# Performance work log

Hardware: AMD Instinct MI355X
Metric: run time of the kernel (lower is better)

Reference implementation:

```python
import jax, jax.numpy as jnp
import numpy as np
import math

B, Q, K, D = 32, 2048, 2048, 128


def setup_inputs() -> dict:
    key = jax.random.key(0)
    k1, k2, k3, k4 = jax.random.split(key, 4)
    return {
        "queries": jax.random.normal(k1, (B, Q, D), dtype=jnp.float32),
        "keys": jax.random.normal(k2, (B, K, D), dtype=jnp.float32),
        "values": jax.random.normal(k3, (B, K, D), dtype=jnp.float32),
        "valid_len": jax.random.randint(k4, (B,), 0, Q, dtype=jnp.int32),
    }


def reference(queries, keys, values, valid_len):
    d = queries.shape[-1]
    # [B, Q, K] scores
    scores = jnp.einsum("bqd,bkd->bqk", queries, keys) / math.sqrt(d)
    # Faithful to source: mask is over the QUERY dim (X.size(1) of [B,Q,K]);
    # rows with q >= valid_len[b] are set entirely to -1e5 before softmax.
    row_mask = jnp.arange(scores.shape[1]) < valid_len[:, None]  # [B, Q]
    scores = jnp.where(row_mask[:, :, None], scores, -100000.0)
    attn = jax.nn.softmax(scores, axis=-1)  # dropout p=0 -> identity
    return jnp.einsum("bqk,bkv->bqv", attn, values)
```

## Files before the change

kernel.cpp:

```cpp
#include <hip/hip_runtime.h>
#include <stdint.h>

#define NB 32
#define NQ 2048
#define NKK 2048
#define DH 128

constexpr int QBLK = 256;
constexpr int KBLK = 64;
constexpr int NKT  = NKK / KBLK;
constexpr float C2 = 0.12754299817f;

typedef short short8  __attribute__((ext_vector_type(8)));
typedef float f32x4   __attribute__((ext_vector_type(4)));
typedef float f32x16  __attribute__((ext_vector_type(16)));
typedef uint32_t u32x4 __attribute__((ext_vector_type(4)));

typedef __attribute__((address_space(3))) uint32_t lds_u32_t;
typedef __attribute__((address_space(1))) const uint32_t glb_u32_t;

__device__ __forceinline__ uint16_t f2bf(float x) {
    union { float f; uint32_t u; } v; v.f = x;
    uint32_t r = v.u + 0x7fffu + ((v.u >> 16) & 1u);
    return (uint16_t)(r >> 16);
}

__device__ __forceinline__ void gload16(const void* g, void* l) {
    __builtin_amdgcn_global_load_lds((glb_u32_t*)g, (lds_u32_t*)l, 16, 0, 0);
}

__device__ __forceinline__ uint32_t cvtpk(float lo, float hi) {
    uint32_t d;
    asm("v_cvt_pk_bf16_f32 %0, %1, %2" : "=v"(d) : "v"(lo), "v"(hi));
    return d;
}

__global__ void conv_kf(const float* __restrict__ K, uint16_t* __restrict__ Kf) {
    __shared__ __align__(16) uint16_t T[64][136];
    const int bid = blockIdx.x;
    const int b = bid >> 5, kt = bid & 31;
    const int tid = threadIdx.x;
    const float* src = K + ((size_t)(b * NKK + kt * 64)) * DH;
    #pragma unroll
    for (int r = 0; r < 8; ++r) {
        int flat = r * 256 + tid;
        int row = flat >> 5;
        int c4 = (flat & 31) * 4;
        f32x4 x = *(const f32x4*)(src + (size_t)row * DH + c4);
        T[row][c4 + 0] = f2bf(x[0]);
        T[row][c4 + 1] = f2bf(x[1]);
        T[row][c4 + 2] = f2bf(x[2]);
        T[row][c4 + 3] = f2bf(x[3]);
    }
    __syncthreads();
    uint16_t* dst = Kf + (size_t)bid * 8192;
    #pragma unroll
    for (int r = 0; r < 4; ++r) {
        int c = r * 256 + tid;
        int s = c >> 6, lane = c & 63;
        int ci = s >> 3, t = s & 7;
        int mm = lane & 31, hh = lane >> 5;
        short8 v = *(const short8*)&T[ci * 32 + mm][t * 16 + hh * 8];
        *(short8*)(dst + (size_t)c * 8) = v;
    }
}

__global__ void conv_vf(const float* __restrict__ V, uint16_t* __restrict__ Vf) {
    const int bid = blockIdx.x;
    const int b = bid >> 5, kt = bid & 31;
    const int tid = threadIdx.x;
    const float* src = V + (size_t)b * NKK * DH;
    uint16_t* dst = Vf + (size_t)bid * 8192;
    #pragma unroll
    for (int r = 0; r < 4; ++r) {
        int c = r * 256 + tid;
        int s = c >> 6, lane = c & 63;
        int ci = s >> 3, nt = (s >> 1) & 3, uu = s & 1;
        int m = lane & 31, h = lane >> 5;
        int kb = kt * 64 + ci * 32 + uu * 16 + 4 * h;
        int d = nt * 32 + m;
        short8 w;
        #pragma unroll
        for (int j = 0; j < 8; ++j) {
            int key = kb + (j & 3) + 8 * (j >> 2);
            w[j] = (short)f2bf(src[(size_t)key * DH + d]);
        }
        *(short8*)(dst + (size_t)c * 8) = w;
    }
}

__global__ __launch_bounds__(256, 1)
void attn_fwd(const float* __restrict__ Qg, const uint16_t* __restrict__ Kf,
              const uint16_t* __restrict__ Vf, const int* __restrict__ VL,
              float* __restrict__ Og) {
    __shared__ __align__(16) uint8_t LB[65536];

    const int tid  = threadIdx.x;
    const int wv   = tid >> 6;
    const int lane = tid & 63;
    const int m    = lane & 31;
    const int h    = lane >> 5;

    const int bid = blockIdx.x;
    const int swz = (bid & 7) * 32 + (bid >> 3);
    const int b   = swz >> 3;
    const int qt  = swz & 7;
    const int qb0 = qt * QBLK + wv * 64;

    const int vlen = VL[b];

    short8 qf[2][8];
    #pragma unroll
    for (int qs = 0; qs < 2; ++qs) {
        const int qrow = qb0 + qs * 32 + m;
        const float qsc = (qrow < vlen) ? C2 : 0.0f;
        const float* qp = Qg + ((size_t)b * NQ + qrow) * DH;
        #pragma unroll
        for (int t = 0; t < 8; ++t) {
            const float* p = qp + t * 16 + h * 8;
            f32x4 x0 = *(const f32x4*)(p);
            f32x4 x1 = *(const f32x4*)(p + 4);
            short8 f;
            f[0] = f2bf(x0[0] * qsc); f[1] = f2bf(x0[1] * qsc);
            f[2] = f2bf(x0[2] * qsc); f[3] = f2bf(x0[3] * qsc);
            f[4] = f2bf(x1[0] * qsc); f[5] = f2bf(x1[1] * qsc);
            f[6] = f2bf(x1[2] * qsc); f[7] = f2bf(x1[3] * qsc);
            qf[qs][t] = f;
        }
    }

    f32x16 oacc[2][4];
    #pragma unroll
    for (int qs = 0; qs < 2; ++qs)
        #pragma unroll
        for (int nt = 0; nt < 4; ++nt)
            #pragma unroll
            for (int r = 0; r < 16; ++r) oacc[qs][nt][r] = 0.0f;
    float lsum[2] = {0.0f, 0.0f};

    const char* kfb = (const char*)Kf + (size_t)b * 32 * 16384;
    const char* vfb = (const char*)Vf + (size_t)b * 32 * 16384;

    auto stage = [&](int buf, int ktile) {
        const char* ks = kfb + (size_t)ktile * 16384;
        const char* vs = vfb + (size_t)ktile * 16384;
        char* kd = (char*)LB + buf * 16384;
        char* vd = (char*)LB + 32768 + buf * 16384;
        #pragma unroll
        for (int r = 0; r < 4; ++r) {
            gload16(ks + r * 4096 + tid * 16, kd + r * 4096 + tid * 16);
            gload16(vs + r * 4096 + tid * 16, vd + r * 4096 + tid * 16);
        }
    };

    stage(0, 0);
    __syncthreads();

    int cur = 0;
    for (int kt = 0; kt < NKT; ++kt) {
        if (kt + 1 < NKT) stage(cur ^ 1, kt + 1);
        const char* KTc = (const char*)LB + cur * 16384 + (size_t)lane * 16;
        const char* VTc = (const char*)LB + 32768 + cur * 16384 + (size_t)lane * 16;

        short8 pa[2][4];
        #pragma unroll
        for (int ci = 0; ci < 2; ++ci) {
            f32x16 s0, s1;
            #pragma unroll
            for (int r = 0; r < 16; ++r) { s0[r] = 0.0f; s1[r] = 0.0f; }
            #pragma unroll
            for (int t = 0; t < 8; ++t) {
                short8 kf = *(const short8*)(KTc + (ci * 8 + t) * 1024);
                s0 = __builtin_amdgcn_mfma_f32_32x32x16_bf16(kf, qf[0][t], s0, 0, 0, 0);
                s1 = __builtin_amdgcn_mfma_f32_32x32x16_bf16(kf, qf[1][t], s1, 0, 0, 0);
            }
            #pragma unroll
            for (int uu = 0; uu < 2; ++uu) {
                float p0[8], p1[8];
                #pragma unroll
                for (int j = 0; j < 8; ++j) {
                    p0[j] = __builtin_amdgcn_exp2f(s0[uu * 8 + j]);
                    p1[j] = __builtin_amdgcn_exp2f(s1[uu * 8 + j]);
                }
                lsum[0] += ((p0[0] + p0[1]) + (p0[2] + p0[3])) + ((p0[4] + p0[5]) + (p0[6] + p0[7]));
                lsum[1] += ((p1[0] + p1[1]) + (p1[2] + p1[3])) + ((p1[4] + p1[5]) + (p1[6] + p1[7]));
                union { uint32_t w[4]; short8 s; } u0, u1;
                u0.w[0] = cvtpk(p0[0], p0[1]); u0.w[1] = cvtpk(p0[2], p0[3]);
                u0.w[2] = cvtpk(p0[4], p0[5]); u0.w[3] = cvtpk(p0[6], p0[7]);
                u1.w[0] = cvtpk(p1[0], p1[1]); u1.w[1] = cvtpk(p1[2], p1[3]);
                u1.w[2] = cvtpk(p1[4], p1[5]); u1.w[3] = cvtpk(p1[6], p1[7]);
                pa[0][ci * 2 + uu] = u0.s;
                pa[1][ci * 2 + uu] = u1.s;
            }
        }

        #pragma unroll
        for (int nt = 0; nt < 4; ++nt) {
            #pragma unroll
            for (int u = 0; u < 4; ++u) {
                const int ci = u >> 1;
                const int uu = u & 1;
                short8 vfr = *(const short8*)(VTc + (ci * 8 + nt * 2 + uu) * 1024);
                oacc[0][nt] = __builtin_amdgcn_mfma_f32_32x32x16_bf16(pa[0][u], vfr, oacc[0][nt], 0, 0, 0);
                oacc[1][nt] = __builtin_amdgcn_mfma_f32_32x32x16_bf16(pa[1][u], vfr, oacc[1][nt], 0, 0, 0);
            }
        }

        __syncthreads();
        cur ^= 1;
    }

    float lt0 = lsum[0] + __shfl_xor(lsum[0], 32);
    float lt1 = lsum[1] + __shfl_xor(lsum[1], 32);
    float* op = Og + ((size_t)b * NQ + qb0) * DH;
    #pragma unroll
    for (int qs = 0; qs < 2; ++qs) {
        float ltq = qs ? lt1 : lt0;
        #pragma unroll
        for (int r = 0; r < 16; ++r) {
            const int qr = (r & 3) + 8 * (r >> 2) + 4 * h;
            float inv = 1.0f / __shfl(ltq, qr);
            #pragma unroll
            for (int nt = 0; nt < 4; ++nt)
                op[(size_t)(qs * 32 + qr) * DH + nt * 32 + m] = oacc[qs][nt][r] * inv;
        }
    }
}

extern "C" void kernel_launch(void* const* d_in, const int* in_sizes, int n_in,
                              void* d_out, int out_size, void* d_ws, size_t ws_size,
                              hipStream_t stream) {
    const float* q  = (const float*)d_in[0];
    const float* k  = (const float*)d_in[1];
    const float* v  = (const float*)d_in[2];
    const int*   vl = (const int*)d_in[3];
    float* out = (float*)d_out;

    uint16_t* Kf = (uint16_t*)d_ws;
    uint16_t* Vf = Kf + (size_t)NB * NKT * 8192;

    conv_kf<<<NB * NKT, 256, 0, stream>>>(k, Kf);
    conv_vf<<<NB * NKT, 256, 0, stream>>>(v, Vf);
    attn_fwd<<<NB * (NQ / QBLK), 256, 0, stream>>>(q, Kf, Vf, vl, out);
}
```

Baseline: 94.76 us.

## Split attention block into compute and producer waves with MFMA priority hints

Raises the block to 512 threads. Four waves do the QK and PV MFMA work, and four dedicated waves only issue the global-to-LDS staging of the next K/V tile. The compute waves also interleave the two key chunks' score MFMAs, reorder the PV loop, and raise wave priority around MFMA sections with s_setprio. The aim is to take load-issue overhead off the compute waves. In exchange, the launch-bounds change to (512,2) can force register spilling given the large accumulator state, and LDS use of 64KB per block may still cap occupancy at one block per CU.

```diff
diff --git a/kernel.cpp b/kernel.cpp
--- a/kernel.cpp
+++ b/kernel.cpp
@@ -89,7 +89,7 @@
     }
 }
 
-__global__ __launch_bounds__(256, 1)
+__global__ __launch_bounds__(512, 2)
 void attn_fwd(const float* __restrict__ Qg, const uint16_t* __restrict__ Kf,
               const uint16_t* __restrict__ Vf, const int* __restrict__ VL,
               float* __restrict__ Og) {
@@ -105,124 +105,142 @@
     const int swz = (bid & 7) * 32 + (bid >> 3);
     const int b   = swz >> 3;
     const int qt  = swz & 7;
-    const int qb0 = qt * QBLK + wv * 64;
-
-    const int vlen = VL[b];
-
-    short8 qf[2][8];
-    #pragma unroll
-    for (int qs = 0; qs < 2; ++qs) {
-        const int qrow = qb0 + qs * 32 + m;
-        const float qsc = (qrow < vlen) ? C2 : 0.0f;
-        const float* qp = Qg + ((size_t)b * NQ + qrow) * DH;
-        #pragma unroll
-        for (int t = 0; t < 8; ++t) {
-            const float* p = qp + t * 16 + h * 8;
-            f32x4 x0 = *(const f32x4*)(p);
-            f32x4 x1 = *(const f32x4*)(p + 4);
-            short8 f;
-            f[0] = f2bf(x0[0] * qsc); f[1] = f2bf(x0[1] * qsc);
-            f[2] = f2bf(x0[2] * qsc); f[3] = f2bf(x0[3] * qsc);
-            f[4] = f2bf(x1[0] * qsc); f[5] = f2bf(x1[1] * qsc);
-            f[6] = f2bf(x1[2] * qsc); f[7] = f2bf(x1[3] * qsc);
-            qf[qs][t] = f;
-        }
-    }
-
-    f32x16 oacc[2][4];
-    #pragma unroll
-    for (int qs = 0; qs < 2; ++qs)
-        #pragma unroll
-        for (int nt = 0; nt < 4; ++nt)
-            #pragma unroll
-            for (int r = 0; r < 16; ++r) oacc[qs][nt][r] = 0.0f;
-    float lsum[2] = {0.0f, 0.0f};
 
     const char* kfb = (const char*)Kf + (size_t)b * 32 * 16384;
     const char* vfb = (const char*)Vf + (size_t)b * 32 * 16384;
 
     auto stage = [&](int buf, int ktile) {
+        const int ptid = tid & 255;
         const char* ks = kfb + (size_t)ktile * 16384;
         const char* vs = vfb + (size_t)ktile * 16384;
         char* kd = (char*)LB + buf * 16384;
         char* vd = (char*)LB + 32768 + buf * 16384;
         #pragma unroll
         for (int r = 0; r < 4; ++r) {
-            gload16(ks + r * 4096 + tid * 16, kd + r * 4096 + tid * 16);
-            gload16(vs + r * 4096 + tid * 16, vd + r * 4096 + tid * 16);
+            gload16(ks + r * 4096 + ptid * 16, kd + r * 4096 + ptid * 16);
+            gload16(vs + r * 4096 + ptid * 16, vd + r * 4096 + ptid * 16);
         }
     };
 
-    stage(0, 0);
+    const int qb0 = qt * QBLK + (wv & 3) * 64;
+
+    short8 qf[2][8];
+    f32x16 oacc[2][4];
+    float lsum[2] = {0.0f, 0.0f};
+
+    if (wv < 4) {
+        const int vlen = VL[b];
+        #pragma unroll
+        for (int qs = 0; qs < 2; ++qs) {
+            const int qrow = qb0 + qs * 32 + m;
+            const float qsc = (qrow < vlen) ? C2 : 0.0f;
+            const float* qp = Qg + ((size_t)b * NQ + qrow) * DH;
+            #pragma unroll
+            for (int t = 0; t < 8; ++t) {
+                const float* p = qp + t * 16 + h * 8;
+                f32x4 x0 = *(const f32x4*)(p);
+                f32x4 x1 = *(const f32x4*)(p + 4);
+                short8 f;
+                f[0] = f2bf(x0[0] * qsc); f[1] = f2bf(x0[1] * qsc);
+                f[2] = f2bf(x0[2] * qsc); f[3] = f2bf(x0[3] * qsc);
+                f[4] = f2bf(x1[0] * qsc); f[5] = f2bf(x1[1] * qsc);
+                f[6] = f2bf(x1[2] * qsc); f[7] = f2bf(x1[3] * qsc);
+                qf[qs][t] = f;
+            }
+        }
+        #pragma unroll
+        for (int qs = 0; qs < 2; ++qs)
+            #pragma unroll
+            for (int nt = 0; nt < 4; ++nt)
+                #pragma unroll
+                for (int r = 0; r < 16; ++r) oacc[qs][nt][r] = 0.0f;
+    } else {
+        stage(0, 0);
+    }
     __syncthreads();
 
-    int cur = 0;
     for (int kt = 0; kt < NKT; ++kt) {
-        if (kt + 1 < NKT) stage(cur ^ 1, kt + 1);
-        const char* KTc = (const char*)LB + cur * 16384 + (size_t)lane * 16;
-        const char* VTc = (const char*)LB + 32768 + cur * 16384 + (size_t)lane * 16;
-
-        short8 pa[2][4];
-        #pragma unroll
-        for (int ci = 0; ci < 2; ++ci) {
-            f32x16 s0, s1;
-            #pragma unroll
-            for (int r = 0; r < 16; ++r) { s0[r] = 0.0f; s1[r] = 0.0f; }
+        const int cur = kt & 1;
+        if (wv < 4) {
+            const char* KTc = (const char*)LB + cur * 16384 + (size_t)lane * 16;
+            const char* VTc = (const char*)LB + 32768 + cur * 16384 + (size_t)lane * 16;
+
+            f32x16 s[2][2];
+            #pragma unroll
+            for (int ci = 0; ci < 2; ++ci)
+                #pragma unroll
+                for (int qs = 0; qs < 2; ++qs)
+                    #pragma unroll
+                    for (int r = 0; r < 16; ++r) s[ci][qs][r] = 0.0f;
+            __builtin_amdgcn_s_setprio(1);
             #pragma unroll
             for (int t = 0; t < 8; ++t) {
-                short8 kf = *(const short8*)(KTc + (ci * 8 + t) * 1024);
-                s0 = __builtin_amdgcn_mfma_f32_32x32x16_bf16(kf, qf[0][t], s0, 0, 0, 0);
-                s1 = __builtin_amdgcn_mfma_f32_32x32x16_bf16(kf, qf[1][t], s1, 0, 0, 0);
-            }
-            #pragma unroll
-            for (int uu = 0; uu < 2; ++uu) {
-                float p0[8], p1[8];
-                #pragma unroll
-                for (int j = 0; j < 8; ++j) {
-                    p0[j] = __builtin_amdgcn_exp2f(s0[uu * 8 + j]);
-                    p1[j] = __builtin_amdgcn_exp2f(s1[uu * 8 + j]);
+                short8 kf0 = *(const short8*)(KTc + (0 * 8 + t) * 1024);
+                short8 kf1 = *(const short8*)(KTc + (1 * 8 + t) * 1024);
+                s[0][0] = __builtin_amdgcn_mfma_f32_32x32x16_bf16(kf0, qf[0][t], s[0][0], 0, 0, 0);
+                s[0][1] = __builtin_amdgcn_mfma_f32_32x32x16_bf16(kf0, qf[1][t], s[0][1], 0, 0, 0);
+                s[1][0] = __builtin_amdgcn_mfma_f32_32x32x16_bf16(kf1, qf[0][t], s[1][0], 0, 0, 0);
+                s[1][1] = __builtin_amdgcn_mfma_f32_32x32x16_bf16(kf1, qf[1][t], s[1][1], 0, 0, 0);
+            }
+            __builtin_amdgcn_s_setprio(0);
+
+            short8 pa[2][4];
+            #pragma unroll
+            for (int ci = 0; ci < 2; ++ci) {
+                #pragma unroll
+                for (int uu = 0; uu < 2; ++uu) {
+                    float p0[8], p1[8];
+                    #pragma unroll
+                    for (int j = 0; j < 8; ++j) {
+                        p0[j] = __builtin_amdgcn_exp2f(s[ci][0][uu * 8 + j]);
+                        p1[j] = __builtin_amdgcn_exp2f(s[ci][1][uu * 8 + j]);
+                    }
+                    lsum[0] += ((p0[0] + p0[1]) + (p0[2] + p0[3])) + ((p0[4] + p0[5]) + (p0[6] + p0[7]));
+                    lsum[1] += ((p1[0] + p1[1]) + (p1[2] + p1[3])) + ((p1[4] + p1[5]) + (p1[6] + p1[7]));
+                    union { uint32_t w[4]; short8 s; } u0, u1;
+                    u0.w[0] = cvtpk(p0[0], p0[1]); u0.w[1] = cvtpk(p0[2], p0[3]);
+                    u0.w[2] = cvtpk(p0[4], p0[5]); u0.w[3] = cvtpk(p0[6], p0[7]);
+                    u1.w[0] = cvtpk(p1[0], p1[1]); u1.w[1] = cvtpk(p1[2], p1[3]);
+                    u1.w[2] = cvtpk(p1[4], p1[5]); u1.w[3] = cvtpk(p1[6], p1[7]);
+                    pa[0][ci * 2 + uu] = u0.s;
+                    pa[1][ci * 2 + uu] = u1.s;
                 }
-                lsum[0] += ((p0[0] + p0[1]) + (p0[2] + p0[3])) + ((p0[4] + p0[5]) + (p0[6] + p0[7]));
-                lsum[1] += ((p1[0] + p1[1]) + (p1[2] + p1[3])) + ((p1[4] + p1[5]) + (p1[6] + p1[7]));
-                union { uint32_t w[4]; short8 s; } u0, u1;
-                u0.w[0] = cvtpk(p0[0], p0[1]); u0.w[1] = cvtpk(p0[2], p0[3]);
-                u0.w[2] = cvtpk(p0[4], p0[5]); u0.w[3] = cvtpk(p0[6], p0[7]);
-                u1.w[0] = cvtpk(p1[0], p1[1]); u1.w[1] = cvtpk(p1[2], p1[3]);
-                u1.w[2] = cvtpk(p1[4], p1[5]); u1.w[3] = cvtpk(p1[6], p1[7]);
-                pa[0][ci * 2 + uu] = u0.s;
-                pa[1][ci * 2 + uu] = u1.s;
-            }
-        }
-
-        #pragma unroll
-        for (int nt = 0; nt < 4; ++nt) {
+            }
+
+            __builtin_amdgcn_s_setprio(1);
             #pragma unroll
             for (int u = 0; u < 4; ++u) {
                 const int ci = u >> 1;
                 const int uu = u & 1;
-                short8 vfr = *(const short8*)(VTc + (ci * 8 + nt * 2 + uu) * 1024);
-                oacc[0][nt] = __builtin_amdgcn_mfma_f32_32x32x16_bf16(pa[0][u], vfr, oacc[0][nt], 0, 0, 0);
-                oacc[1][nt] = __builtin_amdgcn_mfma_f32_32x32x16_bf16(pa[1][u], vfr, oacc[1][nt], 0, 0, 0);
-            }
-        }
-
+                #pragma unroll
+                for (int nt = 0; nt < 4; ++nt) {
+                    short8 vfr = *(const short8*)(VTc + (ci * 8 + nt * 2 + uu) * 1024);
+                    oacc[0][nt] = __builtin_amdgcn_mfma_f32_32x32x16_bf16(pa[0][u], vfr, oacc[0][nt], 0, 0, 0);
+                    oacc[1][nt] = __builtin_amdgcn_mfma_f32_32x32x16_bf16(pa[1][u], vfr, oacc[1][nt], 0, 0, 0);
+                }
+            }
+            __builtin_amdgcn_s_setprio(0);
+        } else if (kt + 1 < NKT) {
+            stage(cur ^ 1, kt + 1);
+        }
         __syncthreads();
-        cur ^= 1;
-    }
-
-    float lt0 = lsum[0] + __shfl_xor(lsum[0], 32);
-    float lt1 = lsum[1] + __shfl_xor(lsum[1], 32);
-    float* op = Og + ((size_t)b * NQ + qb0) * DH;
-    #pragma unroll
-    for (int qs = 0; qs < 2; ++qs) {
-        float ltq = qs ? lt1 : lt0;
-        #pragma unroll
-        for (int r = 0; r < 16; ++r) {
-            const int qr = (r & 3) + 8 * (r >> 2) + 4 * h;
-            float inv = 1.0f / __shfl(ltq, qr);
-            #pragma unroll
-            for (int nt = 0; nt < 4; ++nt)
-                op[(size_t)(qs * 32 + qr) * DH + nt * 32 + m] = oacc[qs][nt][r] * inv;
+    }
+
+    if (wv < 4) {
+        float lt0 = lsum[0] + __shfl_xor(lsum[0], 32);
+        float lt1 = lsum[1] + __shfl_xor(lsum[1], 32);
+        float* op = Og + ((size_t)b * NQ + qb0) * DH;
+        #pragma unroll
+        for (int qs = 0; qs < 2; ++qs) {
+            float ltq = qs ? lt1 : lt0;
+            #pragma unroll
+            for (int r = 0; r < 16; ++r) {
+                const int qr = (r & 3) + 8 * (r >> 2) + 4 * h;
+                float inv = 1.0f / __shfl(ltq, qr);
+                #pragma unroll
+                for (int nt = 0; nt < 4; ++nt)
+                    op[(size_t)(qs * 32 + qr) * DH + nt * 32 + m] = oacc[qs][nt][r] * inv;
+            }
         }
     }
 }
@@ -241,5 +259,5 @@
 
     conv_kf<<<NB * NKT, 256, 0, stream>>>(k, Kf);
     conv_vf<<<NB * NKT, 256, 0, stream>>>(v, Vf);
-    attn_fwd<<<NB * (NQ / QBLK), 256, 0, stream>>>(q, Kf, Vf, vl, out);
-}
+    attn_fwd<<<NB * (NQ / QBLK), 512, 0, stream>>>(q, Kf, Vf, vl, out);
+}
```

New measurement: 118.6 us. +25.2%, slower.
